# Kernel optimization log

Measured on AMD Instinct MI355X. Metric: run time of the kernel, lower is better.

## Reference

```python
import jax, jax.numpy as jnp
import numpy as np

EPS = 1e-5

def _ln(x, g, b):
    m = jnp.mean(x, axis=-1, keepdims=True)
    v = jnp.mean((x - m) ** 2, axis=-1, keepdims=True)
    return (x - m) * jax.lax.rsqrt(v + EPS) * g + b


def setup_inputs() -> dict:
    key = jax.random.key(0)
    B, T, C, H, A = 4, 1024, 1024, 16, 64
    ks = jax.random.split(key, 16)
    s = 0.02
    inp = {
        "x": jax.random.normal(ks[0], (B, T, C), jnp.float32),
        "ln1_g": jnp.ones((C,), jnp.float32), "ln1_b": jnp.zeros((C,), jnp.float32),
        "ln2_g": jnp.ones((C,), jnp.float32), "ln2_b": jnp.zeros((C,), jnp.float32),
        "ln3_g": jnp.ones((C,), jnp.float32), "ln3_b": jnp.zeros((C,), jnp.float32),
        "wq": jax.random.normal(ks[1], (C, C), jnp.float32) * s, "bq": jnp.zeros((C,), jnp.float32),
        "wk": jax.random.normal(ks[2], (C, C), jnp.float32) * s, "bk": jnp.zeros((C,), jnp.float32),
        "wv": jax.random.normal(ks[3], (C, C), jnp.float32) * s, "bv": jnp.zeros((C,), jnp.float32),
        "wo": jax.random.normal(ks[4], (C, C), jnp.float32) * s, "bo": jnp.zeros((C,), jnp.float32),
        "w1": jax.random.normal(ks[5], (C, 4 * C), jnp.float32) * s, "b1": jnp.zeros((4 * C,), jnp.float32),
        "w2": jax.random.normal(ks[6], (4 * C, C), jnp.float32) * s, "b2": jnp.zeros((C,), jnp.float32),
        "wd": jax.random.normal(ks[7], (C, A), jnp.float32) * 1e-4, "bd": jnp.zeros((A,), jnp.float32),
        "wu": jax.random.normal(ks[8], (A, C), jnp.float32) * 1e-4, "bu": jnp.zeros((C,), jnp.float32),
    }
    return inp


def _block(x, ln1_g, ln1_b, ln2_g, ln2_b, ln3_g, ln3_b,
           wq, bq, wk, bk, wv, bv, wo, bo, w1, b1, w2, b2, wd, bd, wu, bu):
    B, T, C = x.shape
    H = 16
    D = C // H
    normed = _ln(x, ln3_g, ln3_b)  # ln3 of original input, used by adapter

    # --- causal self-attention on ln1(x) ---
    h = _ln(x, ln1_g, ln1_b)
    q = (h @ wq + bq).reshape(B, T, H, D)
    k = (h @ wk + bk).reshape(B, T, H, D)
    v = (h @ wv + bv).reshape(B, T, H, D)
    att = jnp.einsum('bqhd,bkhd->bhqk', q, k) * (1.0 / np.sqrt(D))
    causal = jnp.tril(jnp.ones((T, T), bool))
    att = jnp.where(causal, att, -jnp.inf)
    att = jax.nn.softmax(att, axis=-1)
    y = jnp.einsum('bhqk,bkhd->bqhd', att, v).reshape(B, T, C)
    attn_out = y @ wo + bo

    hidden = x + attn_out
    # --- MLP on ln2(hidden) ---
    m = _ln(hidden, ln2_g, ln2_b)
    mlp_out = jax.nn.gelu(m @ w1 + b1, approximate=False) @ w2 + b2
    forward_states = hidden + mlp_out

    # --- adapter on ln3(original x) ---
    a = jax.nn.relu(normed @ wd + bd) @ wu + bu

    # dropout is identity (p=0 / eval)
    return hidden + forward_states + a


def reference(x, ln1_g, ln1_b, ln2_g, ln2_b, ln3_g, ln3_b,
              wq, bq, wk, bk, wv, bv, wo, bo, w1, b1, w2, b2, wd, bd, wu, bu):
    return _block(x, ln1_g, ln1_b, ln2_g, ln2_b, ln3_g, ln3_b,
                  wq, bq, wk, bk, wv, bv, wo, bo, w1, b1, w2, b2, wd, bd, wu, bu)
```

## Files before the change

### kernel.cpp

```cpp
#include <hip/hip_runtime.h>

typedef unsigned short u16;
typedef __bf16 bf16x8 __attribute__((ext_vector_type(8)));
typedef u16    u16x8  __attribute__((ext_vector_type(8)));
typedef float  f32x4  __attribute__((ext_vector_type(4)));

__device__ __forceinline__ u16 f2bf(float f) {
    union { float f; unsigned u; } x{f};
    unsigned r = x.u + 0x7fffu + ((x.u >> 16) & 1u);
    return (u16)(r >> 16);
}
__device__ __forceinline__ float bf2f(u16 h) {
    union { unsigned u; float f; } x{(unsigned)h << 16};
    return x.f;
}

__device__ __forceinline__ f32x4 mfma16(bf16x8 a, bf16x8 b, f32x4 c) {
    return __builtin_amdgcn_mfma_f32_16x16x32_bf16(a, b, c, 0, 0, 0);
}

__device__ __forceinline__ void async_ld16(const void* g, void* l) {
    __builtin_amdgcn_global_load_lds(
        (const __attribute__((address_space(1))) unsigned int*)g,
        (__attribute__((address_space(3))) unsigned int*)l, 16, 0, 0);
}

struct PrepParams {
    const float* src[8];
    u16* dst[8];
    int K[8], N[8];
    int pfx[9];
    const float *bq, *bk, *bv;
    float* bqkv;
    const float *x, *g1, *b1, *g3, *b3;
    u16 *o1, *o3;
};

__global__ void prep_kernel(PrepParams p) {
    const int b = blockIdx.x;
    const int t = threadIdx.x;
    __shared__ float tile[64][65];
    __shared__ float red[8];

    if (b >= p.pfx[8] + 12) {
        const int row = b - p.pfx[8] - 12;
        const long base = (long)row * 1024;
        float4 v = ((const float4*)(p.x + base))[t];
        float s = v.x + v.y + v.z + v.w;
        float ss = v.x * v.x + v.y * v.y + v.z * v.z + v.w * v.w;
        for (int o = 32; o > 0; o >>= 1) { s += __shfl_down(s, o); ss += __shfl_down(ss, o); }
        if ((t & 63) == 0) { red[t >> 6] = s; red[(t >> 6) + 4] = ss; }
        __syncthreads();
        float sum = red[0] + red[1] + red[2] + red[3];
        float sq  = red[4] + red[5] + red[6] + red[7];
        const float mean = sum * (1.f / 1024.f);
        const float rstd = rsqrtf(sq * (1.f / 1024.f) - mean * mean + 1e-5f);
        float4 G1 = ((const float4*)p.g1)[t], B1 = ((const float4*)p.b1)[t];
        float4 G3 = ((const float4*)p.g3)[t], B3 = ((const float4*)p.b3)[t];
        float n0 = (v.x - mean) * rstd, n1 = (v.y - mean) * rstd;
        float n2 = (v.z - mean) * rstd, n3 = (v.w - mean) * rstd;
        ushort4 o1, o3;
        o1.x = f2bf(n0 * G1.x + B1.x); o1.y = f2bf(n1 * G1.y + B1.y);
        o1.z = f2bf(n2 * G1.z + B1.z); o1.w = f2bf(n3 * G1.w + B1.w);
        o3.x = f2bf(n0 * G3.x + B3.x); o3.y = f2bf(n1 * G3.y + B3.y);
        o3.z = f2bf(n2 * G3.z + B3.z); o3.w = f2bf(n3 * G3.w + B3.w);
        ((ushort4*)(p.o1 + base))[t] = o1;
        ((ushort4*)(p.o3 + base))[t] = o3;
        return;
    }
    if (b >= p.pfx[8]) {
        int i = (b - p.pfx[8]) * 256 + t;
        p.bqkv[i] = i < 1024 ? p.bq[i] : (i < 2048 ? p.bk[i - 1024] : p.bv[i - 2048]);
        return;
    }
    int j = 0;
    while (b >= p.pfx[j + 1]) ++j;
    const float* __restrict__ in = p.src[j];
    u16* __restrict__ out = p.dst[j];
    const int K = p.K[j], N = p.N[j];
    const int local = b - p.pfx[j];
    const int tx = N >> 6;
    const int n0 = (local % tx) * 64, k0 = (local / tx) * 64;
    const int rr = t >> 4, cc = t & 15;
#pragma unroll
    for (int it = 0; it < 4; ++it) {
        const int r = rr + it * 16;
        float4 v = *(const float4*)(in + (long)(k0 + r) * N + n0 + cc * 4);
        tile[r][cc * 4 + 0] = v.x; tile[r][cc * 4 + 1] = v.y;
        tile[r][cc * 4 + 2] = v.z; tile[r][cc * 4 + 3] = v.w;
    }
    __syncthreads();
#pragma unroll
    for (int it = 0; it < 4; ++it) {
        const int n = rr + it * 16;
        ushort4 o;
        o.x = f2bf(tile[cc * 4 + 0][n]);
        o.y = f2bf(tile[cc * 4 + 1][n]);
        o.z = f2bf(tile[cc * 4 + 2][n]);
        o.w = f2bf(tile[cc * 4 + 3][n]);
        *(ushort4*)(out + (long)(n0 + n) * K + k0 + cc * 4) = o;
    }
}

__global__ void ln_single_kernel(const float* __restrict__ x,
                                 const float* __restrict__ g, const float* __restrict__ b,
                                 u16* __restrict__ out) {
    const int row = blockIdx.x;
    const long base = (long)row * 1024;
    const int t = threadIdx.x;
    float4 v = ((const float4*)(x + base))[t];
    float s = v.x + v.y + v.z + v.w;
    float ss = v.x * v.x + v.y * v.y + v.z * v.z + v.w * v.w;
    for (int o = 32; o > 0; o >>= 1) { s += __shfl_down(s, o); ss += __shfl_down(ss, o); }
    __shared__ float red[8];
    if ((t & 63) == 0) { red[t >> 6] = s; red[(t >> 6) + 4] = ss; }
    __syncthreads();
    float sum = red[0] + red[1] + red[2] + red[3];
    float sq  = red[4] + red[5] + red[6] + red[7];
    const float mean = sum * (1.f / 1024.f);
    const float rstd = rsqrtf(sq * (1.f / 1024.f) - mean * mean + 1e-5f);
    float4 G = ((const float4*)g)[t], B = ((const float4*)b)[t];
    ushort4 o;
    o.x = f2bf((v.x - mean) * rstd * G.x + B.x);
    o.y = f2bf((v.y - mean) * rstd * G.y + B.y);
    o.z = f2bf((v.z - mean) * rstd * G.z + B.z);
    o.w = f2bf((v.w - mean) * rstd * G.w + B.w);
    ((ushort4*)(out + base))[t] = o;
}

__global__ void transpose_v(const u16* __restrict__ qkv, u16* __restrict__ vT) {
    const int bh = blockIdx.z, b = bh >> 4, hh = bh & 15;
    const int t0 = blockIdx.x * 32, d0 = blockIdx.y * 32;
    __shared__ u16 tile[32][33];
    const u16* src = qkv + (long)(b * 1024) * 3072 + 2048 + hh * 64;
    for (int i = threadIdx.y; i < 32; i += 8)
        tile[i][threadIdx.x] = src[(long)(t0 + i) * 3072 + d0 + threadIdx.x];
    __syncthreads();
    u16* dst = vT + (long)bh * 64 * 1024;
    for (int i = threadIdx.y; i < 32; i += 8)
        dst[(long)(d0 + i) * 1024 + t0 + threadIdx.x] = tile[threadIdx.x][i];
}

__global__ void reduce_out4(float* __restrict__ out, const u16* __restrict__ p,
                            const float* __restrict__ b2) {
    const long base = (long)blockIdx.x * 1024;
    const int t = threadIdx.x;
    float4 sum = {0.f, 0.f, 0.f, 0.f};
#pragma unroll
    for (int z = 0; z < 4; ++z) {
        ushort4 q = ((const ushort4*)(p + (long)z * (4096L * 1024) + base))[t];
        sum.x += bf2f(q.x); sum.y += bf2f(q.y);
        sum.z += bf2f(q.z); sum.w += bf2f(q.w);
    }
    float4 bias = ((const float4*)b2)[t];
    float4 o = ((const float4*)(out + base))[t];
    o.x += sum.x + bias.x; o.y += sum.y + bias.y;
    o.z += sum.z + bias.z; o.w += sum.w + bias.w;
    ((float4*)(out + base))[t] = o;
}

template <typename Epi>
__global__ __launch_bounds__(128, 2)
void gemm_big(const u16* __restrict__ A, const u16* __restrict__ Bt,
              int N, int K, int ld, Epi epi) {
    constexpr int AE = 128 * 32;
    __shared__ u16 sm[2][AE + AE];
    const int tid = threadIdx.x;
    const int wid = tid >> 6, lane = tid & 63;
    const int lr = lane & 15, lh = lane >> 4;

    const int Gx = gridDim.x, Gy = gridDim.y;
    const int id2d = blockIdx.x + Gx * blockIdx.y;
    const int c8 = id2d & 7, l = id2d >> 3;
    const int sx = Gx >> 2;
    const int bx = (c8 & 3) * sx + l % sx;
    const int by = (c8 >> 2) * (Gy >> 1) + l / sx;
    const int m0 = by * 128, n0 = bx * 128;
    const long k0g = (long)blockIdx.z * K;
    const int wn = wid * 64;

    const int cr = lane >> 2, lq = lane & 3;
    long aoff[4], boff[4];
    int lA[4], lB[4];
#pragma unroll
    for (int c = 0; c < 4; ++c) {
        const int r = wid * 64 + c * 16 + cr;
        const int q = lq ^ (r & 3) ^ ((r >> 2) & 3);
        aoff[c] = (long)(m0 + r) * ld + k0g + q * 8;
        boff[c] = (long)(n0 + r) * ld + k0g + q * 8;
        lA[c] = (wid * 4 + c) * 512;
        lB[c] = AE + (wid * 4 + c) * 512;
    }
    const int qoff = ((lh ^ (lr & 3) ^ ((lr >> 2) & 3)) & 3) * 8;

    f32x4 acc[8][4] = {};
    const int nk = K / 32;

    auto stage = [&](int kt) {
        const long ko = (long)kt * 32;
        u16* s = sm[kt & 1];
#pragma unroll
        for (int c = 0; c < 4; ++c) {
            async_ld16(A + aoff[c] + ko, s + lA[c]);
            async_ld16(Bt + boff[c] + ko, s + lB[c]);
        }
    };
    auto compute = [&](int kt) {
        const u16* sA = sm[kt & 1];
        const u16* sB = sA + AE;
        bf16x8 bfr[4];
#pragma unroll
        for (int j = 0; j < 4; ++j)
            bfr[j] = *(const bf16x8*)(sB + (wn + j * 16 + lr) * 32 + qoff);
#pragma unroll
        for (int i = 0; i < 8; ++i) {
            bf16x8 af = *(const bf16x8*)(sA + (i * 16 + lr) * 32 + qoff);
#pragma unroll
            for (int j = 0; j < 4; ++j)
                acc[i][j] = mfma16(af, bfr[j], acc[i][j]);
        }
    };

    stage(0);
    __syncthreads();
    for (int kt = 0; kt < nk; ++kt) {
        if (kt + 1 < nk) stage(kt + 1);
        compute(kt);
        __syncthreads();
    }

#pragma unroll
    for (int i = 0; i < 8; ++i)
#pragma unroll
        for (int j = 0; j < 4; ++j) {
            const int col = n0 + wn + j * 16 + lr;
#pragma unroll
            for (int r = 0; r < 4; ++r)
                epi(m0 + i * 16 + lh * 4 + r, col, acc[i][j][r]);
        }
}

template <typename Epi>
__global__ __launch_bounds__(256, 4)
void gemm_64(const u16* __restrict__ A, const u16* __restrict__ Bt,
             int N, int K, int ld, Epi epi) {
    constexpr int AE = 128 * 32;
    constexpr int BE = 64 * 32;
    __shared__ u16 sm[2][AE + BE];
    const int tid = threadIdx.x;
    const int m0 = blockIdx.y * 128;
    const int n0 = blockIdx.x * 64;
    const long k0g = (long)blockIdx.z * K;
    const int wid = tid >> 6, lane = tid & 63;
    const int lr = lane & 15, lh = lane >> 4;
    const int wm = wid * 32;

    const int cr = lane >> 2, lq = lane & 3;
    const int ra0 = wid * 32 + cr, ra1 = ra0 + 16;
    const int qa0 = lq ^ (ra0 & 3) ^ ((ra0 >> 2) & 3);
    const int qa1 = lq ^ (ra1 & 3) ^ ((ra1 >> 2) & 3);
    const long aoff0 = (long)(m0 + ra0) * ld + k0g + qa0 * 8;
    const long aoff1 = (long)(m0 + ra1) * ld + k0g + qa1 * 8;
    const int la0 = wid * 1024, la1 = la0 + 512;

    const int rb = wid * 16 + cr;
    const int qb = lq ^ (rb & 3) ^ ((rb >> 2) & 3);
    const long boff0 = (long)min(n0 + rb, N - 1) * ld + k0g + qb * 8;
    const int lb0 = AE + wid * 512;

    const int qoff = ((lh ^ (lr & 3) ^ ((lr >> 2) & 3)) & 3) * 8;

    f32x4 acc[2][4] = {};
    const int nk = K / 32;

    auto stage = [&](int kt) {
        const long ko = (long)kt * 32;
        u16* s = sm[kt & 1];
        async_ld16(A + aoff0 + ko, s + la0);
        async_ld16(A + aoff1 + ko, s + la1);
        async_ld16(Bt + boff0 + ko, s + lb0);
    };
    auto compute = [&](int kt) {
        const u16* sA = sm[kt & 1];
        const u16* sB = sA + AE;
        bf16x8 af[2], bfr[4];
#pragma unroll
        for (int i = 0; i < 2; ++i)
            af[i] = *(const bf16x8*)(sA + (wm + i * 16 + lr) * 32 + qoff);
#pragma unroll
        for (int j = 0; j < 4; ++j)
            bfr[j] = *(const bf16x8*)(sB + (j * 16 + lr) * 32 + qoff);
#pragma unroll
        for (int i = 0; i < 2; ++i)
#pragma unroll
            for (int j = 0; j < 4; ++j)
                acc[i][j] = mfma16(af[i], bfr[j], acc[i][j]);
    };

    stage(0);
    __syncthreads();
    for (int kt = 0; kt < nk; ++kt) {
        if (kt + 1 < nk) stage(kt + 1);
        compute(kt);
        __syncthreads();
    }

#pragma unroll
    for (int i = 0; i < 2; ++i)
#pragma unroll
        for (int j = 0; j < 4; ++j) {
            const int col = n0 + j * 16 + lr;
            if (col < N) {
#pragma unroll
                for (int r = 0; r < 4; ++r) {
                    const int row = m0 + wm + i * 16 + lh * 4 + r;
                    epi(row, col, acc[i][j][r]);
                }
            }
        }
}

struct EpiBF16Bias {
    u16* out; const float* bias; int ldo;
    __device__ void operator()(int r, int c, float v) const {
        out[(long)r * ldo + c] = f2bf(v + bias[c]);
    }
};
struct EpiResid {
    float* hidden; const float* bias; const float* x;
    __device__ void operator()(int r, int c, float v) const {
        long i = (long)r * 1024 + c; hidden[i] = v + bias[c] + x[i];
    }
};
struct EpiGelu {
    u16* out; const float* bias;
    __device__ void operator()(int r, int c, float v) const {
        float x = v + bias[c];
        float u2 = x * (1.5957691216f + 0.0713548162726f * x * x);
        float g = x / (1.f + __expf(-u2));
        out[(long)r * 4096 + c] = f2bf(g);
    }
};
struct EpiReluBF16 {
    u16* out; const float* bias;
    __device__ void operator()(int r, int c, float v) const {
        out[(long)r * 64 + c] = f2bf(fmaxf(v + bias[c], 0.f));
    }
};
struct EpiAdapter {
    float* out; const float* bias; const float* hidden;
    __device__ void operator()(int r, int c, float v) const {
        long i = (long)r * 1024 + c; out[i] = 2.f * hidden[i] + v + bias[c];
    }
};
struct EpiStoreSplit {
    u16* p;
    __device__ void operator()(int r, int c, float v) const {
        p[(long)blockIdx.z * (4096L * 1024) + (long)r * 1024 + c] = f2bf(v);
    }
};

__global__ __launch_bounds__(256, 2)
void attn_kernel(const u16* __restrict__ qkv, const u16* __restrict__ vT,
                 u16* __restrict__ y) {
    const int bh = blockIdx.x, b = bh >> 4, hh = bh & 15;
    const int q0 = blockIdx.y * 128;
    const int tid = threadIdx.x, wid = tid >> 6, lane = tid & 63;
    const int lr = lane & 15, lh = lane >> 4;
    const int qw = q0 + wid * 32;

    __shared__ u16 smK[64 * 72];
    __shared__ u16 smV[64 * 72];
    __shared__ u16 smP[4 * 32 * 72];
    u16* pw = smP + wid * (32 * 72);

    const u16* qbase = qkv + (long)(b * 1024) * 3072 + hh * 64;
    const u16* kbase = qbase + 1024;
    const u16* vbase = vT + (long)bh * 64 * 1024;

    bf16x8 a_q[2][2];
#pragma unroll
    for (int mt = 0; mt < 2; ++mt)
#pragma unroll
        for (int ks = 0; ks < 2; ++ks) {
            uint4 t = *(const uint4*)(qbase + (long)(qw + mt * 16 + lr) * 3072 + ks * 32 + lh * 8);
            a_q[mt][ks] = __builtin_bit_cast(bf16x8, t);
        }

    bf16x8 ones;
    { u16x8 t = {0x3F80, 0x3F80, 0x3F80, 0x3F80, 0x3F80, 0x3F80, 0x3F80, 0x3F80};
      ones = __builtin_bit_cast(bf16x8, t); }

    f32x4 o_acc[2][4] = {};
    f32x4 l_acc[2] = {};
    f32x4 m_run[2] = {{-1e30f, -1e30f, -1e30f, -1e30f}, {-1e30f, -1e30f, -1e30f, -1e30f}};

    const int ntiles = q0 / 64 + 2;
    const int ck = tid >> 3, cs = (tid & 7) * 8;
    const int ck2 = (tid + 256) >> 3, cs2 = ((tid + 256) & 7) * 8;
    for (int kt = 0; kt < ntiles; ++kt) {
        const int k0 = kt * 64;
        __syncthreads();
        {
            uint4 kv0 = *(const uint4*)(kbase + (long)(k0 + ck) * 3072 + cs);
            uint4 kv1 = *(const uint4*)(kbase + (long)(k0 + ck2) * 3072 + cs2);
            *(uint4*)(smK + ck * 72 + cs) = kv0;
            *(uint4*)(smK + ck2 * 72 + cs2) = kv1;
            uint4 vv0 = *(const uint4*)(vbase + (long)ck * 1024 + k0 + cs);
            uint4 vv1 = *(const uint4*)(vbase + (long)ck2 * 1024 + k0 + cs2);
            *(uint4*)(smV + ck * 72 + cs) = vv0;
            *(uint4*)(smV + ck2 * 72 + cs2) = vv1;
        }
        __syncthreads();
        if (k0 > qw + 31) continue;

        bf16x8 bK[4][2];
#pragma unroll
        for (int nt = 0; nt < 4; ++nt)
#pragma unroll
            for (int ks = 0; ks < 2; ++ks)
                bK[nt][ks] = *(const bf16x8*)(smK + (nt * 16 + lr) * 72 + ks * 32 + lh * 8);

        f32x4 s[2][4];
#pragma unroll
        for (int mt = 0; mt < 2; ++mt)
#pragma unroll
            for (int nt = 0; nt < 4; ++nt) {
                f32x4 z = {0.f, 0.f, 0.f, 0.f};
                z = mfma16(a_q[mt][0], bK[nt][0], z);
                z = mfma16(a_q[mt][1], bK[nt][1], z);
                s[mt][nt] = z;
            }
#pragma unroll
        for (int mt = 0; mt < 2; ++mt) {
            const int qb = qw + mt * 16 + lh * 4;
#pragma unroll
            for (int nt = 0; nt < 4; ++nt) {
                const int kkg = k0 + nt * 16 + lr;
#pragma unroll
                for (int r = 0; r < 4; ++r) {
                    float v = s[mt][nt][r] * 0.125f;
                    if (kkg > qb + r) v = -1e30f;
                    s[mt][nt][r] = v;
                }
            }
        }
#pragma unroll
        for (int mt = 0; mt < 2; ++mt) {
            f32x4 mx = s[mt][0];
#pragma unroll
            for (int nt = 1; nt < 4; ++nt)
#pragma unroll
                for (int r = 0; r < 4; ++r) mx[r] = fmaxf(mx[r], s[mt][nt][r]);
#pragma unroll
            for (int xm = 1; xm < 16; xm <<= 1)
#pragma unroll
                for (int r = 0; r < 4; ++r) mx[r] = fmaxf(mx[r], __shfl_xor(mx[r], xm));
            f32x4 mnew, alpha;
#pragma unroll
            for (int r = 0; r < 4; ++r) {
                mnew[r] = fmaxf(m_run[mt][r], mx[r]);
                alpha[r] = __expf(m_run[mt][r] - mnew[r]);
            }
            m_run[mt] = mnew;
            l_acc[mt] *= alpha;
#pragma unroll
            for (int dt = 0; dt < 4; ++dt) o_acc[mt][dt] *= alpha;
#pragma unroll
            for (int nt = 0; nt < 4; ++nt)
#pragma unroll
                for (int r = 0; r < 4; ++r)
                    s[mt][nt][r] = __expf(s[mt][nt][r] - mnew[r]);
#pragma unroll
            for (int nt = 0; nt < 4; ++nt)
#pragma unroll
                for (int r = 0; r < 4; ++r)
                    pw[(mt * 16 + lh * 4 + r) * 72 + nt * 16 + lr] = f2bf(s[mt][nt][r]);
        }
        bf16x8 vf[4][2];
#pragma unroll
        for (int dt = 0; dt < 4; ++dt)
#pragma unroll
            for (int ks = 0; ks < 2; ++ks)
                vf[dt][ks] = *(const bf16x8*)(smV + (dt * 16 + lr) * 72 + ks * 32 + lh * 8);
#pragma unroll
        for (int mt = 0; mt < 2; ++mt) {
            bf16x8 pf0 = *(const bf16x8*)(pw + (mt * 16 + lr) * 72 + lh * 8);
            bf16x8 pf1 = *(const bf16x8*)(pw + (mt * 16 + lr) * 72 + 32 + lh * 8);
            l_acc[mt] = mfma16(pf0, ones, l_acc[mt]);
            l_acc[mt] = mfma16(pf1, ones, l_acc[mt]);
#pragma unroll
            for (int dt = 0; dt < 4; ++dt) {
                o_acc[mt][dt] = mfma16(pf0, vf[dt][0], o_acc[mt][dt]);
                o_acc[mt][dt] = mfma16(pf1, vf[dt][1], o_acc[mt][dt]);
            }
        }
    }
#pragma unroll
    for (int mt = 0; mt < 2; ++mt) {
        f32x4 linv;
#pragma unroll
        for (int r = 0; r < 4; ++r) linv[r] = 1.f / l_acc[mt][r];
#pragma unroll
        for (int dt = 0; dt < 4; ++dt) {
#pragma unroll
            for (int r = 0; r < 4; ++r) {
                const int tok = b * 1024 + qw + mt * 16 + lh * 4 + r;
                y[(long)tok * 1024 + hh * 64 + dt * 16 + lr] = f2bf(o_acc[mt][dt][r] * linv[r]);
            }
        }
    }
}

extern "C" void kernel_launch(void* const* d_in, const int* in_sizes, int n_in,
                              void* d_out, int out_size, void* d_ws, size_t ws_size,
                              hipStream_t stream) {
    const float* x    = (const float*)d_in[0];
    const float* ln1g = (const float*)d_in[1];
    const float* ln1b = (const float*)d_in[2];
    const float* ln2g = (const float*)d_in[3];
    const float* ln2b = (const float*)d_in[4];
    const float* ln3g = (const float*)d_in[5];
    const float* ln3b = (const float*)d_in[6];
    const float* wq = (const float*)d_in[7];  const float* bq = (const float*)d_in[8];
    const float* wk = (const float*)d_in[9];  const float* bk = (const float*)d_in[10];
    const float* wv = (const float*)d_in[11]; const float* bv = (const float*)d_in[12];
    const float* wo = (const float*)d_in[13]; const float* bo = (const float*)d_in[14];
    const float* w1 = (const float*)d_in[15]; const float* b1 = (const float*)d_in[16];
    const float* w2 = (const float*)d_in[17]; const float* b2 = (const float*)d_in[18];
    const float* wd = (const float*)d_in[19]; const float* bd = (const float*)d_in[20];
    const float* wu = (const float*)d_in[21]; const float* bu = (const float*)d_in[22];
    float* out = (float*)d_out;

    char* base = (char*)d_ws;
    size_t off = 0;
    auto carve = [&](size_t bytes) -> char* {
        char* p = base + off; off += (bytes + 255) & ~(size_t)255; return p;
    };
    u16* qkv_wt = (u16*)carve(3072L * 1024 * 2);
    u16* wo_t   = (u16*)carve(1024L * 1024 * 2);
    u16* w1_t   = (u16*)carve(4096L * 1024 * 2);
    u16* w2_t   = (u16*)carve(1024L * 4096 * 2);
    u16* wd_t   = (u16*)carve(64L * 1024 * 2);
    u16* wu_t   = (u16*)carve(1024L * 64 * 2);
    float* bqkv = (float*)carve(3072L * 4);
    u16* hbuf   = (u16*)carve(4096L * 1024 * 2);
    u16* nrm    = (u16*)carve(4096L * 1024 * 2);
    u16* qkvb   = (u16*)carve(4096L * 3072 * 2);
    u16* vT     = (u16*)carve(64L * 64 * 1024 * 2);
    u16* ybuf   = (u16*)carve(4096L * 1024 * 2);
    float* hid  = (float*)carve(4096L * 1024 * 4);
    u16* mbuf   = (u16*)carve(4096L * 1024 * 2);
    u16* act    = (u16*)carve(4096L * 4096 * 2);
    u16* t1     = (u16*)carve(4096L * 64 * 2);
    u16* part   = (u16*)carve(4L * 4096 * 1024 * 2);

    PrepParams pp;
    pp.src[0] = wq; pp.dst[0] = qkv_wt;                 pp.K[0] = 1024; pp.N[0] = 1024;
    pp.src[1] = wk; pp.dst[1] = qkv_wt + 1024L * 1024;  pp.K[1] = 1024; pp.N[1] = 1024;
    pp.src[2] = wv; pp.dst[2] = qkv_wt + 2048L * 1024;  pp.K[2] = 1024; pp.N[2] = 1024;
    pp.src[3] = wo; pp.dst[3] = wo_t;                   pp.K[3] = 1024; pp.N[3] = 1024;
    pp.src[4] = w1; pp.dst[4] = w1_t;                   pp.K[4] = 1024; pp.N[4] = 4096;
    pp.src[5] = w2; pp.dst[5] = w2_t;                   pp.K[5] = 4096; pp.N[5] = 1024;
    pp.src[6] = wd; pp.dst[6] = wd_t;                   pp.K[6] = 1024; pp.N[6] = 64;
    pp.src[7] = wu; pp.dst[7] = wu_t;                   pp.K[7] = 64;   pp.N[7] = 1024;
    int acc_blocks = 0;
    for (int j = 0; j < 8; ++j) {
        pp.pfx[j] = acc_blocks;
        acc_blocks += (pp.N[j] >> 6) * (pp.K[j] >> 6);
    }
    pp.pfx[8] = acc_blocks;
    pp.bq = bq; pp.bk = bk; pp.bv = bv; pp.bqkv = bqkv;
    pp.x = x; pp.g1 = ln1g; pp.b1 = ln1b; pp.g3 = ln3g; pp.b3 = ln3b;
    pp.o1 = hbuf; pp.o3 = nrm;
    prep_kernel<<<acc_blocks + 12 + 4096, 256, 0, stream>>>(pp);

    gemm_big<<<dim3(24, 32), 128, 0, stream>>>(hbuf, qkv_wt, 3072, 1024, 1024,
                                               EpiBF16Bias{qkvb, bqkv, 3072});
    transpose_v<<<dim3(32, 2, 64), dim3(32, 8), 0, stream>>>(qkvb, vT);
    attn_kernel<<<dim3(64, 8), 256, 0, stream>>>(qkvb, vT, ybuf);
    gemm_64<<<dim3(16, 32), 256, 0, stream>>>(ybuf, wo_t, 1024, 1024, 1024,
                                              EpiResid{hid, bo, x});
    ln_single_kernel<<<4096, 256, 0, stream>>>(hid, ln2g, ln2b, mbuf);
    gemm_big<<<dim3(32, 32), 128, 0, stream>>>(mbuf, w1_t, 4096, 1024, 1024,
                                               EpiGelu{act, b1});
    gemm_64<<<dim3(1, 32), 256, 0, stream>>>(nrm, wd_t, 64, 1024, 1024,
                                             EpiReluBF16{t1, bd});
    gemm_64<<<dim3(16, 32), 256, 0, stream>>>(t1, wu_t, 1024, 64, 64,
                                              EpiAdapter{out, bu, hid});
    gemm_big<<<dim3(8, 32, 4), 128, 0, stream>>>(act, w2_t, 1024, 1024, 4096,
                                                 EpiStoreSplit{part});
    reduce_out4<<<4096, 256, 0, stream>>>(out, part, b2);
}
```

Measured before the change: 392.8 us.

## Pre-pack B weights into MFMA fragment layout and load B directly to registers

The weight prep kernel now writes the QKV, W1 and W2 matrices in a packed layout matching the 16x16x32 MFMA B-fragment order. gemm_big then loads B fragments straight from global memory into double-buffered registers instead of staging them through LDS, which halves LDS use and drops the B LDS reads. The QKV GEMM is split into three launches because the packed layout is per-matrix. The cost is more global traffic per wave, since each wave reads its own B without sharing through LDS, plus register pressure from holding two fragment buffers.

```diff
diff --git a/kernel.cpp b/kernel.cpp
--- a/kernel.cpp
+++ b/kernel.cpp
@@ -28,7 +28,7 @@
 struct PrepParams {
     const float* src[8];
     u16* dst[8];
-    int K[8], N[8];
+    int K[8], N[8], pack[8];
     int pfx[9];
     const float *bq, *bk, *bv;
     float* bqkv;
@@ -90,6 +90,7 @@
         tile[r][cc * 4 + 2] = v.z; tile[r][cc * 4 + 3] = v.w;
     }
     __syncthreads();
+    const int nT16 = N >> 4;
 #pragma unroll
     for (int it = 0; it < 4; ++it) {
         const int n = rr + it * 16;
@@ -98,7 +99,14 @@
         o.y = f2bf(tile[cc * 4 + 1][n]);
         o.z = f2bf(tile[cc * 4 + 2][n]);
         o.w = f2bf(tile[cc * 4 + 3][n]);
-        *(ushort4*)(out + (long)(n0 + n) * K + k0 + cc * 4) = o;
+        if (p.pack[j]) {
+            const int gn = n0 + n, gk = k0 + cc * 4;
+            long idx = ((long)((gk >> 5) * nT16 + (gn >> 4)) * 64 +
+                        ((gn & 15) + ((gk >> 3) & 3) * 16)) * 8 + (gk & 7);
+            *(ushort4*)(out + idx) = o;
+        } else {
+            *(ushort4*)(out + (long)(n0 + n) * K + k0 + cc * 4) = o;
+        }
     }
 }
 
@@ -161,10 +169,10 @@
 
 template <typename Epi>
 __global__ __launch_bounds__(128, 2)
-void gemm_big(const u16* __restrict__ A, const u16* __restrict__ Bt,
-              int N, int K, int ld, Epi epi) {
+void gemm_big(const u16* __restrict__ A, const u16* __restrict__ Bp,
+              int nT16, int K, int ld, Epi epi) {
     constexpr int AE = 128 * 32;
-    __shared__ u16 sm[2][AE + AE];
+    __shared__ u16 sm[2][AE];
     const int tid = threadIdx.x;
     const int wid = tid >> 6, lane = tid & 63;
     const int lr = lane & 15, lh = lane >> 4;
@@ -177,19 +185,19 @@
     const int by = (c8 >> 2) * (Gy >> 1) + l / sx;
     const int m0 = by * 128, n0 = bx * 128;
     const long k0g = (long)blockIdx.z * K;
+    const int kt0 = (int)(k0g >> 5);
+    const int jt0 = (n0 >> 4) + wid * 4;
     const int wn = wid * 64;
 
     const int cr = lane >> 2, lq = lane & 3;
-    long aoff[4], boff[4];
-    int lA[4], lB[4];
+    long aoff[4];
+    int lA[4];
 #pragma unroll
     for (int c = 0; c < 4; ++c) {
         const int r = wid * 64 + c * 16 + cr;
         const int q = lq ^ (r & 3) ^ ((r >> 2) & 3);
         aoff[c] = (long)(m0 + r) * ld + k0g + q * 8;
-        boff[c] = (long)(n0 + r) * ld + k0g + q * 8;
         lA[c] = (wid * 4 + c) * 512;
-        lB[c] = AE + (wid * 4 + c) * 512;
     }
     const int qoff = ((lh ^ (lr & 3) ^ ((lr >> 2) & 3)) & 3) * 8;
 
@@ -200,18 +208,17 @@
         const long ko = (long)kt * 32;
         u16* s = sm[kt & 1];
 #pragma unroll
-        for (int c = 0; c < 4; ++c) {
+        for (int c = 0; c < 4; ++c)
             async_ld16(A + aoff[c] + ko, s + lA[c]);
-            async_ld16(Bt + boff[c] + ko, s + lB[c]);
-        }
     };
-    auto compute = [&](int kt) {
+    auto load_b = [&](bf16x8* bfr, int kt) {
+        const long bbase = ((long)(kt0 + kt) * nT16 + jt0) * 512 + lane * 8;
+#pragma unroll
+        for (int j = 0; j < 4; ++j)
+            bfr[j] = *(const bf16x8*)(Bp + bbase + j * 512);
+    };
+    auto compute = [&](int kt, bf16x8* bfr) {
         const u16* sA = sm[kt & 1];
-        const u16* sB = sA + AE;
-        bf16x8 bfr[4];
-#pragma unroll
-        for (int j = 0; j < 4; ++j)
-            bfr[j] = *(const bf16x8*)(sB + (wn + j * 16 + lr) * 32 + qoff);
 #pragma unroll
         for (int i = 0; i < 8; ++i) {
             bf16x8 af = *(const bf16x8*)(sA + (i * 16 + lr) * 32 + qoff);
@@ -221,11 +228,16 @@
         }
     };
 
+    bf16x8 b0[4], b1[4];
     stage(0);
+    load_b(b0, 0);
     __syncthreads();
     for (int kt = 0; kt < nk; ++kt) {
-        if (kt + 1 < nk) stage(kt + 1);
-        compute(kt);
+        if (kt + 1 < nk) {
+            stage(kt + 1);
+            load_b((kt & 1) ? b0 : b1, kt + 1);
+        }
+        compute(kt, (kt & 1) ? b1 : b0);
         __syncthreads();
     }
 
@@ -556,14 +568,14 @@
     u16* part   = (u16*)carve(4L * 4096 * 1024 * 2);
 
     PrepParams pp;
-    pp.src[0] = wq; pp.dst[0] = qkv_wt;                 pp.K[0] = 1024; pp.N[0] = 1024;
-    pp.src[1] = wk; pp.dst[1] = qkv_wt + 1024L * 1024;  pp.K[1] = 1024; pp.N[1] = 1024;
-    pp.src[2] = wv; pp.dst[2] = qkv_wt + 2048L * 1024;  pp.K[2] = 1024; pp.N[2] = 1024;
-    pp.src[3] = wo; pp.dst[3] = wo_t;                   pp.K[3] = 1024; pp.N[3] = 1024;
-    pp.src[4] = w1; pp.dst[4] = w1_t;                   pp.K[4] = 1024; pp.N[4] = 4096;
-    pp.src[5] = w2; pp.dst[5] = w2_t;                   pp.K[5] = 4096; pp.N[5] = 1024;
-    pp.src[6] = wd; pp.dst[6] = wd_t;                   pp.K[6] = 1024; pp.N[6] = 64;
-    pp.src[7] = wu; pp.dst[7] = wu_t;                   pp.K[7] = 64;   pp.N[7] = 1024;
+    pp.src[0] = wq; pp.dst[0] = qkv_wt;                 pp.K[0] = 1024; pp.N[0] = 1024; pp.pack[0] = 1;
+    pp.src[1] = wk; pp.dst[1] = qkv_wt + 1024L * 1024;  pp.K[1] = 1024; pp.N[1] = 1024; pp.pack[1] = 1;
+    pp.src[2] = wv; pp.dst[2] = qkv_wt + 2048L * 1024;  pp.K[2] = 1024; pp.N[2] = 1024; pp.pack[2] = 1;
+    pp.src[3] = wo; pp.dst[3] = wo_t;                   pp.K[3] = 1024; pp.N[3] = 1024; pp.pack[3] = 0;
+    pp.src[4] = w1; pp.dst[4] = w1_t;                   pp.K[4] = 1024; pp.N[4] = 4096; pp.pack[4] = 1;
+    pp.src[5] = w2; pp.dst[5] = w2_t;                   pp.K[5] = 4096; pp.N[5] = 1024; pp.pack[5] = 1;
+    pp.src[6] = wd; pp.dst[6] = wd_t;                   pp.K[6] = 1024; pp.N[6] = 64;   pp.pack[6] = 0;
+    pp.src[7] = wu; pp.dst[7] = wu_t;                   pp.K[7] = 64;   pp.N[7] = 1024; pp.pack[7] = 0;
     int acc_blocks = 0;
     for (int j = 0; j < 8; ++j) {
         pp.pfx[j] = acc_blocks;
@@ -575,20 +587,24 @@
     pp.o1 = hbuf; pp.o3 = nrm;
     prep_kernel<<<acc_blocks + 12 + 4096, 256, 0, stream>>>(pp);
 
-    gemm_big<<<dim3(24, 32), 128, 0, stream>>>(hbuf, qkv_wt, 3072, 1024, 1024,
-                                               EpiBF16Bias{qkvb, bqkv, 3072});
+    gemm_big<<<dim3(8, 32), 128, 0, stream>>>(hbuf, qkv_wt, 64, 1024, 1024,
+                                              EpiBF16Bias{qkvb, bqkv, 3072});
+    gemm_big<<<dim3(8, 32), 128, 0, stream>>>(hbuf, qkv_wt + 1024L * 1024, 64, 1024, 1024,
+                                              EpiBF16Bias{qkvb + 1024, bqkv + 1024, 3072});
+    gemm_big<<<dim3(8, 32), 128, 0, stream>>>(hbuf, qkv_wt + 2048L * 1024, 64, 1024, 1024,
+                                              EpiBF16Bias{qkvb + 2048, bqkv + 2048, 3072});
     transpose_v<<<dim3(32, 2, 64), dim3(32, 8), 0, stream>>>(qkvb, vT);
     attn_kernel<<<dim3(64, 8), 256, 0, stream>>>(qkvb, vT, ybuf);
     gemm_64<<<dim3(16, 32), 256, 0, stream>>>(ybuf, wo_t, 1024, 1024, 1024,
                                               EpiResid{hid, bo, x});
     ln_single_kernel<<<4096, 256, 0, stream>>>(hid, ln2g, ln2b, mbuf);
-    gemm_big<<<dim3(32, 32), 128, 0, stream>>>(mbuf, w1_t, 4096, 1024, 1024,
+    gemm_big<<<dim3(32, 32), 128, 0, stream>>>(mbuf, w1_t, 256, 1024, 1024,
                                                EpiGelu{act, b1});
     gemm_64<<<dim3(1, 32), 256, 0, stream>>>(nrm, wd_t, 64, 1024, 1024,
                                              EpiReluBF16{t1, bd});
     gemm_64<<<dim3(16, 32), 256, 0, stream>>>(t1, wu_t, 1024, 64, 64,
                                               EpiAdapter{out, bu, hid});
-    gemm_big<<<dim3(8, 32, 4), 128, 0, stream>>>(act, w2_t, 1024, 1024, 4096,
+    gemm_big<<<dim3(8, 32, 4), 128, 0, stream>>>(act, w2_t, 64, 1024, 4096,
                                                  EpiStoreSplit{part});
     reduce_out4<<<4096, 256, 0, stream>>>(out, part, b2);
 }
```

Result: slower. 489.5 us (+24.6%).
